# Kernel optimization log

Hardware: AMD Instinct MI355X
Metric: run time of the kernel (lower is better)

## Reference

```python
import jax, jax.numpy as jnp
import numpy as np
from math import sqrt

B, L, S, H, E = 4, 2048, 2048, 16, 64


def setup_inputs() -> dict:
    key = jax.random.key(0)
    kq, kk, kv = jax.random.split(key, 3)
    queries = jax.random.normal(kq, (B, L, H, E), dtype=jnp.float32)
    keys = jax.random.normal(kk, (B, S, H, E), dtype=jnp.float32)
    values = jax.random.normal(kv, (B, S, H, E), dtype=jnp.float32)
    # causal mask: True where attention is disallowed (upper triangle, excl diag)
    causal = jnp.triu(jnp.ones((L, S), dtype=jnp.bool_), k=1)
    attention_mask = jnp.broadcast_to(causal[None, None, :, :], (B, 1, L, S))
    return {"queries": queries, "keys": keys, "values": values,
            "attention_mask": attention_mask}


def reference(queries, keys, values, attention_mask):
    E_ = queries.shape[-1]
    scale = 1.0 / sqrt(E_)
    # [B,H,L,S] full score matrix (the quadratic intermediate of naive attention)
    scores = jnp.einsum('blhe,bshe->bhls', queries, keys)
    scores = jnp.where(attention_mask, -jnp.inf, scores)
    A = jnp.nan_to_num(jax.nn.softmax(scale * scores, axis=-1))
    V = jnp.einsum('bhls,bshd->blhd', A, values)
    return V
```

## Files before the change

kernel.cpp:

```cpp
#include <hip/hip_runtime.h>
#include <cmath>

#define B_ 4
#define L_ 2048
#define S_ 2048
#define H_ 16
#define E_ 64
#define SCALE 0.125f

typedef __attribute__((ext_vector_type(4))) float f32x4;
typedef __attribute__((ext_vector_type(8))) __bf16 bf16x8;
typedef __attribute__((ext_vector_type(8))) unsigned short ushort8;
typedef __attribute__((ext_vector_type(4))) unsigned short ushort4v;
union FragU { ushort8 u; bf16x8 b; };

__device__ __forceinline__ unsigned short f2bf(float f) {
    unsigned int u = __float_as_uint(f);
    return (unsigned short)((u + 0x7FFFu + ((u >> 16) & 1u)) >> 16);
}

__device__ __forceinline__ void gload_lds16(const void* g, void* l) {
    __builtin_amdgcn_global_load_lds(
        (const __attribute__((address_space(1))) void*)g,
        (__attribute__((address_space(3))) void*)l, 16, 0, 0);
}

__global__ __launch_bounds__(256) void conv_k(const float* __restrict__ K,
                                              unsigned short* __restrict__ Kbf) {
    const int idx = blockIdx.x * 256 + threadIdx.x;
    const int j   = idx & 7;
    const int row = idx >> 3;
    const int s   = row & (S_ - 1);
    const int bh  = row >> 11;
    const int h   = bh & (H_ - 1);
    const int b   = bh >> 4;
    const int jp  = j ^ (s & 7);
    const float* src = K + (((size_t)b * S_ + s) * H_ + h) * E_ + jp * 8;
    f32x4 a = *(const f32x4*)src;
    f32x4 d = *(const f32x4*)(src + 4);
    ushort8 u;
    u[0]=f2bf(a[0]); u[1]=f2bf(a[1]); u[2]=f2bf(a[2]); u[3]=f2bf(a[3]);
    u[4]=f2bf(d[0]); u[5]=f2bf(d[1]); u[6]=f2bf(d[2]); u[7]=f2bf(d[3]);
    *(ushort8*)(Kbf + (size_t)row * E_ + j * 8) = u;
}

__global__ __launch_bounds__(256) void conv_v(const float* __restrict__ V,
                                              unsigned short* __restrict__ Vt) {
    __shared__ unsigned short t[64 * 72];
    const int tid  = threadIdx.x;
    const int sblk = blockIdx.x & 31;
    const int h    = (blockIdx.x >> 5) & 15;
    const int b    = blockIdx.x >> 9;
    const int s0   = sblk * 64;
    for (int i = 0; i < 4; ++i) {
        const int c = tid + i * 256;
        const int sr = c >> 4, e0 = (c & 15) * 4;
        f32x4 a = *(const f32x4*)(V + (((size_t)b * S_ + s0 + sr) * H_ + h) * E_ + e0);
        ushort4v u;
        u[0]=f2bf(a[0]); u[1]=f2bf(a[1]); u[2]=f2bf(a[2]); u[3]=f2bf(a[3]);
        *(ushort4v*)&t[sr * 72 + e0] = u;
    }
    __syncthreads();
    for (int i = 0; i < 2; ++i) {
        const int c = tid + i * 256;
        const int e = c >> 3, lc = c & 7, sch = lc ^ (e & 7);
        ushort8 u;
        for (int k = 0; k < 8; ++k) u[k] = t[(sch * 8 + k) * 72 + e];
        *(ushort8*)(Vt + ((size_t)(b * H_ + h) * E_ + e) * S_ + s0 + lc * 8) = u;
    }
}

template <bool PRE>
__global__ __launch_bounds__(256, 6) void fattn_kernel(
    const float* __restrict__ Q, const unsigned short* __restrict__ Kbf,
    const unsigned short* __restrict__ Vt, const float* __restrict__ Kf,
    const float* __restrict__ Vf, float* __restrict__ Out)
{
    const int tid  = threadIdx.x;
    const int wave = tid >> 6;
    const int lane = tid & 63;
    const int ln   = lane & 15;
    const int quad = lane >> 4;
    const int qtile = gridDim.x - 1 - blockIdx.x;
    const int h = blockIdx.y;
    const int b = blockIdx.z;
    const int q0 = qtile * 64;
    const int qw = q0 + wave * 16;
    const int p7 = ln & 7;

    __shared__ __align__(16) unsigned short ldsK[64 * 64];
    __shared__ __align__(16) unsigned short ldsV[64 * 64];
    __shared__ __align__(16) unsigned short ldsP[4][16 * 72];

    FragU qf[2];
    {
        const float* qp = Q + (((size_t)b * L_ + (qw + ln)) * H_ + h) * E_;
        for (int c = 0; c < 2; ++c) {
            const int e0 = c * 32 + quad * 8;
            f32x4 lo = *(const f32x4*)(qp + e0);
            f32x4 hi = *(const f32x4*)(qp + e0 + 4);
            ushort8 u;
            u[0]=f2bf(lo[0]*SCALE); u[1]=f2bf(lo[1]*SCALE);
            u[2]=f2bf(lo[2]*SCALE); u[3]=f2bf(lo[3]*SCALE);
            u[4]=f2bf(hi[0]*SCALE); u[5]=f2bf(hi[1]*SCALE);
            u[6]=f2bf(hi[2]*SCALE); u[7]=f2bf(hi[3]*SCALE);
            qf[c].u = u;
        }
    }

    f32x4 o[4];
    for (int et = 0; et < 4; ++et) o[et] = f32x4{0.f, 0.f, 0.f, 0.f};
    float l_r[4] = {0.f, 0.f, 0.f, 0.f};

    const unsigned short* kbh = Kbf + (size_t)(b * H_ + h) * S_ * E_;
    const unsigned short* vbh = Vt  + (size_t)(b * H_ + h) * E_ * S_;
    const float* kf32 = Kf + (((size_t)b * S_) * H_ + h) * E_;
    const float* vf32 = Vf + (((size_t)b * S_) * H_ + h) * E_;

    const int ntiles = qtile + 1;
    for (int kt = 0; kt < ntiles; ++kt) {
        const int k0 = kt * 64;
        __syncthreads();

        if constexpr (PRE) {
            const unsigned short* ktb = kbh + (size_t)k0 * E_;
            const unsigned short* vtb = vbh + k0;
            for (int i = 0; i < 2; ++i) {
                const int slot0 = wave * 128 + i * 64;
                gload_lds16(ktb + (size_t)(slot0 + lane) * 8, &ldsK[slot0 * 8]);
            }
            for (int i = 0; i < 2; ++i) {
                const int slot0 = wave * 128 + i * 64;
                const int slot  = slot0 + lane;
                const int e = slot >> 3, lc = slot & 7;
                gload_lds16(vtb + (size_t)e * S_ + lc * 8, &ldsV[slot0 * 8]);
            }
        } else {
            for (int i = 0; i < 2; ++i) {
                const int c = tid + i * 256;
                const int key = c >> 3, j = c & 7, jp = j ^ (key & 7);
                const float* src = kf32 + (size_t)(k0 + key) * (H_ * E_) + jp * 8;
                f32x4 a = *(const f32x4*)src, d = *(const f32x4*)(src + 4);
                ushort8 u;
                u[0]=f2bf(a[0]); u[1]=f2bf(a[1]); u[2]=f2bf(a[2]); u[3]=f2bf(a[3]);
                u[4]=f2bf(d[0]); u[5]=f2bf(d[1]); u[6]=f2bf(d[2]); u[7]=f2bf(d[3]);
                *(ushort8*)&ldsK[key * 64 + j * 8] = u;
            }
            for (int i = 0; i < 2; ++i) {
                const int c = tid + i * 256;
                const int e = c >> 3, lc = c & 7, sch = lc ^ (e & 7);
                ushort8 u;
                for (int t = 0; t < 8; ++t)
                    u[t] = f2bf(vf32[(size_t)(k0 + sch * 8 + t) * (H_ * E_) + e]);
                *(ushort8*)&ldsV[e * 64 + lc * 8] = u;
            }
        }
        __syncthreads();

        f32x4 sfr[4];
        for (int n = 0; n < 4; ++n) {
            FragU kf0, kf1;
            kf0.u = *(const ushort8*)&ldsK[(n*16+ln)*64 + ((quad    ) ^ p7) * 8];
            kf1.u = *(const ushort8*)&ldsK[(n*16+ln)*64 + ((4 + quad) ^ p7) * 8];
            f32x4 acc = f32x4{0.f, 0.f, 0.f, 0.f};
            acc = __builtin_amdgcn_mfma_f32_16x16x32_bf16(qf[0].b, kf0.b, acc, 0, 0, 0);
            acc = __builtin_amdgcn_mfma_f32_16x16x32_bf16(qf[1].b, kf1.b, acc, 0, 0, 0);
            sfr[n] = acc;
        }

        for (int r = 0; r < 4; ++r) {
            const int qrow = qw + quad * 4 + r;
            for (int n = 0; n < 4; ++n) {
                const int col = k0 + n * 16 + ln;
                float p = __expf(sfr[n][r]);
                p = (col <= qrow) ? p : 0.f;
                l_r[r] += p;
                ldsP[wave][(quad * 4 + r) * 72 + n * 16 + ln] = f2bf(p);
            }
        }

        FragU pf0, pf1;
        pf0.u = *(const ushort8*)&ldsP[wave][ln * 72 + quad * 8];
        pf1.u = *(const ushort8*)&ldsP[wave][ln * 72 + 32 + quad * 8];
        for (int et = 0; et < 4; ++et) {
            FragU vf0, vf1;
            vf0.u = *(const ushort8*)&ldsV[(et*16+ln)*64 + ((quad    ) ^ p7) * 8];
            vf1.u = *(const ushort8*)&ldsV[(et*16+ln)*64 + ((4 + quad) ^ p7) * 8];
            o[et] = __builtin_amdgcn_mfma_f32_16x16x32_bf16(pf0.b, vf0.b, o[et], 0, 0, 0);
            o[et] = __builtin_amdgcn_mfma_f32_16x16x32_bf16(pf1.b, vf1.b, o[et], 0, 0, 0);
        }
    }

    for (int r = 0; r < 4; ++r) {
        float s = l_r[r];
        s += __shfl_xor(s, 1); s += __shfl_xor(s, 2);
        s += __shfl_xor(s, 4); s += __shfl_xor(s, 8);
        l_r[r] = s;
    }

    for (int r = 0; r < 4; ++r) {
        const float inv = 1.f / l_r[r];
        const int qrow = qw + quad * 4 + r;
        float* op = Out + (((size_t)b * L_ + qrow) * H_ + h) * E_;
        for (int et = 0; et < 4; ++et)
            op[et * 16 + ln] = o[et][r] * inv;
    }
}

extern "C" void kernel_launch(void* const* d_in, const int* in_sizes, int n_in,
                              void* d_out, int out_size, void* d_ws, size_t ws_size,
                              hipStream_t stream) {
    const float* Q = (const float*)d_in[0];
    const float* K = (const float*)d_in[1];
    const float* V = (const float*)d_in[2];
    float* Out = (float*)d_out;

    const size_t plane = (size_t)B_ * H_ * S_ * E_;
    unsigned short* Kbf = (unsigned short*)d_ws;
    unsigned short* Vt  = Kbf + plane;

    dim3 grid(L_ / 64, H_, B_);
    if (ws_size >= plane * 2 * sizeof(unsigned short)) {
        conv_k<<<(int)(plane / 8 / 256), 256, 0, stream>>>(K, Kbf);
        conv_v<<<B_ * H_ * (S_ / 64), 256, 0, stream>>>(V, Vt);
        fattn_kernel<true><<<grid, dim3(256), 0, stream>>>(Q, Kbf, Vt, K, V, Out);
    } else {
        fattn_kernel<false><<<grid, dim3(256), 0, stream>>>(Q, Kbf, Vt, K, V, Out);
    }
}
```

Baseline: 277.7 us.

## Double-buffer K tiles in LDS and load V fragments directly from global

K tiles are now prefetched into a double-buffered LDS array one tile ahead, which removes one of the two barriers per iteration. V fragments are read straight from global memory into registers instead of being staged through LDS, so the V transpose kernel drops its XOR swizzle. Softmax now uses exp2 with log2(e) folded into the Q scale, and the occupancy hint drops from 6 to 4 waves per SIMD to allow more registers. The direct global V loads are strided and repeated by every wave, and correctness relies on the asynchronous LDS loads finishing before the barrier.

```diff
diff --git a/kernel.cpp b/kernel.cpp
--- a/kernel.cpp
+++ b/kernel.cpp
@@ -6,7 +6,7 @@
 #define S_ 2048
 #define H_ 16
 #define E_ 64
-#define SCALE 0.125f
+#define SCALE2 0.18033688011112042f
 
 typedef __attribute__((ext_vector_type(4))) float f32x4;
 typedef __attribute__((ext_vector_type(8))) __bf16 bf16x8;
@@ -46,7 +46,7 @@
 
 __global__ __launch_bounds__(256) void conv_v(const float* __restrict__ V,
                                               unsigned short* __restrict__ Vt) {
-    __shared__ unsigned short t[64 * 72];
+    __shared__ unsigned short t[64 * 65];
     const int tid  = threadIdx.x;
     const int sblk = blockIdx.x & 31;
     const int h    = (blockIdx.x >> 5) & 15;
@@ -56,22 +56,23 @@
         const int c = tid + i * 256;
         const int sr = c >> 4, e0 = (c & 15) * 4;
         f32x4 a = *(const f32x4*)(V + (((size_t)b * S_ + s0 + sr) * H_ + h) * E_ + e0);
-        ushort4v u;
-        u[0]=f2bf(a[0]); u[1]=f2bf(a[1]); u[2]=f2bf(a[2]); u[3]=f2bf(a[3]);
-        *(ushort4v*)&t[sr * 72 + e0] = u;
+        t[sr * 65 + e0 + 0] = f2bf(a[0]);
+        t[sr * 65 + e0 + 1] = f2bf(a[1]);
+        t[sr * 65 + e0 + 2] = f2bf(a[2]);
+        t[sr * 65 + e0 + 3] = f2bf(a[3]);
     }
     __syncthreads();
     for (int i = 0; i < 2; ++i) {
         const int c = tid + i * 256;
-        const int e = c >> 3, lc = c & 7, sch = lc ^ (e & 7);
+        const int e = c >> 3, lc = c & 7;
         ushort8 u;
-        for (int k = 0; k < 8; ++k) u[k] = t[(sch * 8 + k) * 72 + e];
+        for (int k = 0; k < 8; ++k) u[k] = t[(lc * 8 + k) * 65 + e];
         *(ushort8*)(Vt + ((size_t)(b * H_ + h) * E_ + e) * S_ + s0 + lc * 8) = u;
     }
 }
 
 template <bool PRE>
-__global__ __launch_bounds__(256, 6) void fattn_kernel(
+__global__ __launch_bounds__(256, 4) void fattn_kernel(
     const float* __restrict__ Q, const unsigned short* __restrict__ Kbf,
     const unsigned short* __restrict__ Vt, const float* __restrict__ Kf,
     const float* __restrict__ Vf, float* __restrict__ Out)
@@ -88,8 +89,7 @@
     const int qw = q0 + wave * 16;
     const int p7 = ln & 7;
 
-    __shared__ __align__(16) unsigned short ldsK[64 * 64];
-    __shared__ __align__(16) unsigned short ldsV[64 * 64];
+    __shared__ __align__(16) unsigned short kbuf[2][64 * 64];
     __shared__ __align__(16) unsigned short ldsP[4][16 * 72];
 
     FragU qf[2];
@@ -100,10 +100,10 @@
             f32x4 lo = *(const f32x4*)(qp + e0);
             f32x4 hi = *(const f32x4*)(qp + e0 + 4);
             ushort8 u;
-            u[0]=f2bf(lo[0]*SCALE); u[1]=f2bf(lo[1]*SCALE);
-            u[2]=f2bf(lo[2]*SCALE); u[3]=f2bf(lo[3]*SCALE);
-            u[4]=f2bf(hi[0]*SCALE); u[5]=f2bf(hi[1]*SCALE);
-            u[6]=f2bf(hi[2]*SCALE); u[7]=f2bf(hi[3]*SCALE);
+            u[0]=f2bf(lo[0]*SCALE2); u[1]=f2bf(lo[1]*SCALE2);
+            u[2]=f2bf(lo[2]*SCALE2); u[3]=f2bf(lo[3]*SCALE2);
+            u[4]=f2bf(hi[0]*SCALE2); u[5]=f2bf(hi[1]*SCALE2);
+            u[6]=f2bf(hi[2]*SCALE2); u[7]=f2bf(hi[3]*SCALE2);
             qf[c].u = u;
         }
     }
@@ -118,23 +118,35 @@
     const float* vf32 = Vf + (((size_t)b * S_) * H_ + h) * E_;
 
     const int ntiles = qtile + 1;
+
+    if constexpr (PRE) {
+        const unsigned short* ktb = kbh;
+        for (int i = 0; i < 2; ++i) {
+            const int slot0 = wave * 128 + i * 64;
+            gload_lds16(ktb + (size_t)(slot0 + lane) * 8, &kbuf[0][slot0 * 8]);
+        }
+    }
+
     for (int kt = 0; kt < ntiles; ++kt) {
         const int k0 = kt * 64;
         __syncthreads();
 
+        FragU vf[4][2];
+        const unsigned short* kb;
         if constexpr (PRE) {
-            const unsigned short* ktb = kbh + (size_t)k0 * E_;
-            const unsigned short* vtb = vbh + k0;
-            for (int i = 0; i < 2; ++i) {
-                const int slot0 = wave * 128 + i * 64;
-                gload_lds16(ktb + (size_t)(slot0 + lane) * 8, &ldsK[slot0 * 8]);
-            }
-            for (int i = 0; i < 2; ++i) {
-                const int slot0 = wave * 128 + i * 64;
-                const int slot  = slot0 + lane;
-                const int e = slot >> 3, lc = slot & 7;
-                gload_lds16(vtb + (size_t)e * S_ + lc * 8, &ldsV[slot0 * 8]);
-            }
+            if (kt + 1 < ntiles) {
+                const unsigned short* ktb = kbh + (size_t)(k0 + 64) * E_;
+                unsigned short* dst = kbuf[(kt + 1) & 1];
+                for (int i = 0; i < 2; ++i) {
+                    const int slot0 = wave * 128 + i * 64;
+                    gload_lds16(ktb + (size_t)(slot0 + lane) * 8, &dst[slot0 * 8]);
+                }
+            }
+            for (int et = 0; et < 4; ++et)
+                for (int hf = 0; hf < 2; ++hf)
+                    vf[et][hf].u = *(const ushort8*)(
+                        vbh + (size_t)(et * 16 + ln) * S_ + k0 + hf * 32 + quad * 8);
+            kb = kbuf[kt & 1];
         } else {
             for (int i = 0; i < 2; ++i) {
                 const int c = tid + i * 256;
@@ -144,24 +156,33 @@
                 ushort8 u;
                 u[0]=f2bf(a[0]); u[1]=f2bf(a[1]); u[2]=f2bf(a[2]); u[3]=f2bf(a[3]);
                 u[4]=f2bf(d[0]); u[5]=f2bf(d[1]); u[6]=f2bf(d[2]); u[7]=f2bf(d[3]);
-                *(ushort8*)&ldsK[key * 64 + j * 8] = u;
-            }
-            for (int i = 0; i < 2; ++i) {
-                const int c = tid + i * 256;
-                const int e = c >> 3, lc = c & 7, sch = lc ^ (e & 7);
-                ushort8 u;
-                for (int t = 0; t < 8; ++t)
-                    u[t] = f2bf(vf32[(size_t)(k0 + sch * 8 + t) * (H_ * E_) + e]);
-                *(ushort8*)&ldsV[e * 64 + lc * 8] = u;
-            }
-        }
-        __syncthreads();
+                *(ushort8*)&kbuf[0][key * 64 + j * 8] = u;
+            }
+            {
+                const int s = tid & 63;
+                const int eb = (tid >> 6) * 16;
+                const float* vp = vf32 + (size_t)(k0 + s) * (H_ * E_) + eb;
+                for (int i = 0; i < 4; ++i) {
+                    f32x4 v4 = *(const f32x4*)(vp + i * 4);
+                    kbuf[1][(eb + i * 4 + 0) * 64 + s] = f2bf(v4[0]);
+                    kbuf[1][(eb + i * 4 + 1) * 64 + s] = f2bf(v4[1]);
+                    kbuf[1][(eb + i * 4 + 2) * 64 + s] = f2bf(v4[2]);
+                    kbuf[1][(eb + i * 4 + 3) * 64 + s] = f2bf(v4[3]);
+                }
+            }
+            __syncthreads();
+            for (int et = 0; et < 4; ++et)
+                for (int hf = 0; hf < 2; ++hf)
+                    vf[et][hf].u = *(const ushort8*)
+                        &kbuf[1][(et * 16 + ln) * 64 + hf * 32 + quad * 8];
+            kb = kbuf[0];
+        }
 
         f32x4 sfr[4];
         for (int n = 0; n < 4; ++n) {
             FragU kf0, kf1;
-            kf0.u = *(const ushort8*)&ldsK[(n*16+ln)*64 + ((quad    ) ^ p7) * 8];
-            kf1.u = *(const ushort8*)&ldsK[(n*16+ln)*64 + ((4 + quad) ^ p7) * 8];
+            kf0.u = *(const ushort8*)&kb[(n*16+ln)*64 + ((quad    ) ^ p7) * 8];
+            kf1.u = *(const ushort8*)&kb[(n*16+ln)*64 + ((4 + quad) ^ p7) * 8];
             f32x4 acc = f32x4{0.f, 0.f, 0.f, 0.f};
             acc = __builtin_amdgcn_mfma_f32_16x16x32_bf16(qf[0].b, kf0.b, acc, 0, 0, 0);
             acc = __builtin_amdgcn_mfma_f32_16x16x32_bf16(qf[1].b, kf1.b, acc, 0, 0, 0);
@@ -172,7 +193,7 @@
             const int qrow = qw + quad * 4 + r;
             for (int n = 0; n < 4; ++n) {
                 const int col = k0 + n * 16 + ln;
-                float p = __expf(sfr[n][r]);
+                float p = __builtin_exp2f(sfr[n][r]);
                 p = (col <= qrow) ? p : 0.f;
                 l_r[r] += p;
                 ldsP[wave][(quad * 4 + r) * 72 + n * 16 + ln] = f2bf(p);
@@ -183,11 +204,8 @@
         pf0.u = *(const ushort8*)&ldsP[wave][ln * 72 + quad * 8];
         pf1.u = *(const ushort8*)&ldsP[wave][ln * 72 + 32 + quad * 8];
         for (int et = 0; et < 4; ++et) {
-            FragU vf0, vf1;
-            vf0.u = *(const ushort8*)&ldsV[(et*16+ln)*64 + ((quad    ) ^ p7) * 8];
-            vf1.u = *(const ushort8*)&ldsV[(et*16+ln)*64 + ((4 + quad) ^ p7) * 8];
-            o[et] = __builtin_amdgcn_mfma_f32_16x16x32_bf16(pf0.b, vf0.b, o[et], 0, 0, 0);
-            o[et] = __builtin_amdgcn_mfma_f32_16x16x32_bf16(pf1.b, vf1.b, o[et], 0, 0, 0);
+            o[et] = __builtin_amdgcn_mfma_f32_16x16x32_bf16(pf0.b, vf[et][0].b, o[et], 0, 0, 0);
+            o[et] = __builtin_amdgcn_mfma_f32_16x16x32_bf16(pf1.b, vf[et][1].b, o[et], 0, 0, 0);
         }
     }
 
@@ -197,7 +215,6 @@
         s += __shfl_xor(s, 4); s += __shfl_xor(s, 8);
         l_r[r] = s;
     }
-
     for (int r = 0; r < 4; ++r) {
         const float inv = 1.f / l_r[r];
         const int qrow = qw + quad * 4 + r;
```

Result: slower. 427.3 us (+53.9%).

## Enlarge query tile to 128 rows per block and skip fully-masked tiles

Applied to the files above, without the earlier changes.

Each wave now handles 32 query rows, so each block covers 128 queries and every K/V tile loaded into LDS is reused by twice as many rows. Waves skip key tiles that lie entirely above their causal diagonal and apply the mask only on diagonal tiles. Softmax uses exp2 with the log2(e) factor folded into the Q scale, and the row sum accumulates the bf16-truncated probabilities so it matches the values fed to the PV matmul. The grid is halved with occupancy lowered to 4 blocks per CU, which risks less latency hiding and more imbalance across waves within a block; the V transpose buffer padding was also changed.

```diff
diff --git a/kernel.cpp b/kernel.cpp
--- a/kernel.cpp
+++ b/kernel.cpp
@@ -6,12 +6,11 @@
 #define S_ 2048
 #define H_ 16
 #define E_ 64
-#define SCALE 0.125f
+#define SCALE2 0.18033688011112042f
 
 typedef __attribute__((ext_vector_type(4))) float f32x4;
 typedef __attribute__((ext_vector_type(8))) __bf16 bf16x8;
 typedef __attribute__((ext_vector_type(8))) unsigned short ushort8;
-typedef __attribute__((ext_vector_type(4))) unsigned short ushort4v;
 union FragU { ushort8 u; bf16x8 b; };
 
 __device__ __forceinline__ unsigned short f2bf(float f) {
@@ -46,7 +45,7 @@
 
 __global__ __launch_bounds__(256) void conv_v(const float* __restrict__ V,
                                               unsigned short* __restrict__ Vt) {
-    __shared__ unsigned short t[64 * 72];
+    __shared__ unsigned short t[64 * 65];
     const int tid  = threadIdx.x;
     const int sblk = blockIdx.x & 31;
     const int h    = (blockIdx.x >> 5) & 15;
@@ -56,22 +55,23 @@
         const int c = tid + i * 256;
         const int sr = c >> 4, e0 = (c & 15) * 4;
         f32x4 a = *(const f32x4*)(V + (((size_t)b * S_ + s0 + sr) * H_ + h) * E_ + e0);
-        ushort4v u;
-        u[0]=f2bf(a[0]); u[1]=f2bf(a[1]); u[2]=f2bf(a[2]); u[3]=f2bf(a[3]);
-        *(ushort4v*)&t[sr * 72 + e0] = u;
+        t[sr * 65 + e0 + 0] = f2bf(a[0]);
+        t[sr * 65 + e0 + 1] = f2bf(a[1]);
+        t[sr * 65 + e0 + 2] = f2bf(a[2]);
+        t[sr * 65 + e0 + 3] = f2bf(a[3]);
     }
     __syncthreads();
     for (int i = 0; i < 2; ++i) {
         const int c = tid + i * 256;
         const int e = c >> 3, lc = c & 7, sch = lc ^ (e & 7);
         ushort8 u;
-        for (int k = 0; k < 8; ++k) u[k] = t[(sch * 8 + k) * 72 + e];
+        for (int k = 0; k < 8; ++k) u[k] = t[(sch * 8 + k) * 65 + e];
         *(ushort8*)(Vt + ((size_t)(b * H_ + h) * E_ + e) * S_ + s0 + lc * 8) = u;
     }
 }
 
 template <bool PRE>
-__global__ __launch_bounds__(256, 6) void fattn_kernel(
+__global__ __launch_bounds__(256, 4) void fattn_kernel(
     const float* __restrict__ Q, const unsigned short* __restrict__ Kbf,
     const unsigned short* __restrict__ Vt, const float* __restrict__ Kf,
     const float* __restrict__ Vf, float* __restrict__ Out)
@@ -84,40 +84,41 @@
     const int qtile = gridDim.x - 1 - blockIdx.x;
     const int h = blockIdx.y;
     const int b = blockIdx.z;
-    const int q0 = qtile * 64;
-    const int qw = q0 + wave * 16;
+    const int q0 = qtile * 128;
+    const int qw = q0 + wave * 32;
     const int p7 = ln & 7;
 
     __shared__ __align__(16) unsigned short ldsK[64 * 64];
     __shared__ __align__(16) unsigned short ldsV[64 * 64];
-    __shared__ __align__(16) unsigned short ldsP[4][16 * 72];
-
-    FragU qf[2];
-    {
-        const float* qp = Q + (((size_t)b * L_ + (qw + ln)) * H_ + h) * E_;
+    __shared__ __align__(16) unsigned short ldsP[4][32 * 72];
+
+    FragU qf[2][2];
+    for (int rs = 0; rs < 2; ++rs) {
+        const float* qp = Q + (((size_t)b * L_ + (qw + rs * 16 + ln)) * H_ + h) * E_;
         for (int c = 0; c < 2; ++c) {
             const int e0 = c * 32 + quad * 8;
             f32x4 lo = *(const f32x4*)(qp + e0);
             f32x4 hi = *(const f32x4*)(qp + e0 + 4);
             ushort8 u;
-            u[0]=f2bf(lo[0]*SCALE); u[1]=f2bf(lo[1]*SCALE);
-            u[2]=f2bf(lo[2]*SCALE); u[3]=f2bf(lo[3]*SCALE);
-            u[4]=f2bf(hi[0]*SCALE); u[5]=f2bf(hi[1]*SCALE);
-            u[6]=f2bf(hi[2]*SCALE); u[7]=f2bf(hi[3]*SCALE);
-            qf[c].u = u;
-        }
-    }
-
-    f32x4 o[4];
-    for (int et = 0; et < 4; ++et) o[et] = f32x4{0.f, 0.f, 0.f, 0.f};
-    float l_r[4] = {0.f, 0.f, 0.f, 0.f};
+            u[0]=f2bf(lo[0]*SCALE2); u[1]=f2bf(lo[1]*SCALE2);
+            u[2]=f2bf(lo[2]*SCALE2); u[3]=f2bf(lo[3]*SCALE2);
+            u[4]=f2bf(hi[0]*SCALE2); u[5]=f2bf(hi[1]*SCALE2);
+            u[6]=f2bf(hi[2]*SCALE2); u[7]=f2bf(hi[3]*SCALE2);
+            qf[rs][c].u = u;
+        }
+    }
+
+    f32x4 o[2][4];
+    for (int rs = 0; rs < 2; ++rs)
+        for (int et = 0; et < 4; ++et) o[rs][et] = f32x4{0.f, 0.f, 0.f, 0.f};
+    float l_r[2][4] = {{0.f,0.f,0.f,0.f},{0.f,0.f,0.f,0.f}};
 
     const unsigned short* kbh = Kbf + (size_t)(b * H_ + h) * S_ * E_;
     const unsigned short* vbh = Vt  + (size_t)(b * H_ + h) * E_ * S_;
     const float* kf32 = Kf + (((size_t)b * S_) * H_ + h) * E_;
     const float* vf32 = Vf + (((size_t)b * S_) * H_ + h) * E_;
 
-    const int ntiles = qtile + 1;
+    const int ntiles = 2 * qtile + 2;
     for (int kt = 0; kt < ntiles; ++kt) {
         const int k0 = kt * 64;
         __syncthreads();
@@ -157,53 +158,66 @@
         }
         __syncthreads();
 
-        f32x4 sfr[4];
+        if (k0 > qw + 31) continue;
+        const bool need_mask = (k0 + 63 > qw);
+
+        f32x4 sfr[2][4];
         for (int n = 0; n < 4; ++n) {
             FragU kf0, kf1;
             kf0.u = *(const ushort8*)&ldsK[(n*16+ln)*64 + ((quad    ) ^ p7) * 8];
             kf1.u = *(const ushort8*)&ldsK[(n*16+ln)*64 + ((4 + quad) ^ p7) * 8];
-            f32x4 acc = f32x4{0.f, 0.f, 0.f, 0.f};
-            acc = __builtin_amdgcn_mfma_f32_16x16x32_bf16(qf[0].b, kf0.b, acc, 0, 0, 0);
-            acc = __builtin_amdgcn_mfma_f32_16x16x32_bf16(qf[1].b, kf1.b, acc, 0, 0, 0);
-            sfr[n] = acc;
-        }
-
-        for (int r = 0; r < 4; ++r) {
-            const int qrow = qw + quad * 4 + r;
-            for (int n = 0; n < 4; ++n) {
-                const int col = k0 + n * 16 + ln;
-                float p = __expf(sfr[n][r]);
-                p = (col <= qrow) ? p : 0.f;
-                l_r[r] += p;
-                ldsP[wave][(quad * 4 + r) * 72 + n * 16 + ln] = f2bf(p);
-            }
-        }
-
-        FragU pf0, pf1;
-        pf0.u = *(const ushort8*)&ldsP[wave][ln * 72 + quad * 8];
-        pf1.u = *(const ushort8*)&ldsP[wave][ln * 72 + 32 + quad * 8];
+            for (int rs = 0; rs < 2; ++rs) {
+                f32x4 acc = f32x4{0.f, 0.f, 0.f, 0.f};
+                acc = __builtin_amdgcn_mfma_f32_16x16x32_bf16(qf[rs][0].b, kf0.b, acc, 0, 0, 0);
+                acc = __builtin_amdgcn_mfma_f32_16x16x32_bf16(qf[rs][1].b, kf1.b, acc, 0, 0, 0);
+                sfr[rs][n] = acc;
+            }
+        }
+
+        for (int rs = 0; rs < 2; ++rs) {
+            for (int r = 0; r < 4; ++r) {
+                const int qrow = qw + rs * 16 + quad * 4 + r;
+                for (int n = 0; n < 4; ++n) {
+                    float p = __builtin_exp2f(sfr[rs][n][r]);
+                    if (need_mask) {
+                        const int col = k0 + n * 16 + ln;
+                        p = (col <= qrow) ? p : 0.f;
+                    }
+                    const unsigned int u = __float_as_uint(p) & 0xFFFF0000u;
+                    l_r[rs][r] += __uint_as_float(u);
+                    ldsP[wave][(rs * 16 + quad * 4 + r) * 72 + n * 16 + ln] =
+                        (unsigned short)(u >> 16);
+                }
+            }
+        }
+
+        FragU pf[2][2];
+        for (int rs = 0; rs < 2; ++rs) {
+            pf[rs][0].u = *(const ushort8*)&ldsP[wave][(rs*16+ln) * 72 + quad * 8];
+            pf[rs][1].u = *(const ushort8*)&ldsP[wave][(rs*16+ln) * 72 + 32 + quad * 8];
+        }
         for (int et = 0; et < 4; ++et) {
             FragU vf0, vf1;
             vf0.u = *(const ushort8*)&ldsV[(et*16+ln)*64 + ((quad    ) ^ p7) * 8];
             vf1.u = *(const ushort8*)&ldsV[(et*16+ln)*64 + ((4 + quad) ^ p7) * 8];
-            o[et] = __builtin_amdgcn_mfma_f32_16x16x32_bf16(pf0.b, vf0.b, o[et], 0, 0, 0);
-            o[et] = __builtin_amdgcn_mfma_f32_16x16x32_bf16(pf1.b, vf1.b, o[et], 0, 0, 0);
-        }
-    }
-
-    for (int r = 0; r < 4; ++r) {
-        float s = l_r[r];
-        s += __shfl_xor(s, 1); s += __shfl_xor(s, 2);
-        s += __shfl_xor(s, 4); s += __shfl_xor(s, 8);
-        l_r[r] = s;
-    }
-
-    for (int r = 0; r < 4; ++r) {
-        const float inv = 1.f / l_r[r];
-        const int qrow = qw + quad * 4 + r;
-        float* op = Out + (((size_t)b * L_ + qrow) * H_ + h) * E_;
-        for (int et = 0; et < 4; ++et)
-            op[et * 16 + ln] = o[et][r] * inv;
+            for (int rs = 0; rs < 2; ++rs) {
+                o[rs][et] = __builtin_amdgcn_mfma_f32_16x16x32_bf16(pf[rs][0].b, vf0.b, o[rs][et], 0, 0, 0);
+                o[rs][et] = __builtin_amdgcn_mfma_f32_16x16x32_bf16(pf[rs][1].b, vf1.b, o[rs][et], 0, 0, 0);
+            }
+        }
+    }
+
+    for (int rs = 0; rs < 2; ++rs) {
+        for (int r = 0; r < 4; ++r) {
+            float s = l_r[rs][r];
+            s += __shfl_xor(s, 1); s += __shfl_xor(s, 2);
+            s += __shfl_xor(s, 4); s += __shfl_xor(s, 8);
+            const float inv = 1.f / s;
+            const int qrow = qw + rs * 16 + quad * 4 + r;
+            float* op = Out + (((size_t)b * L_ + qrow) * H_ + h) * E_;
+            for (int et = 0; et < 4; ++et)
+                op[et * 16 + ln] = o[rs][et][r] * inv;
+        }
     }
 }
 
@@ -219,7 +233,7 @@
     unsigned short* Kbf = (unsigned short*)d_ws;
     unsigned short* Vt  = Kbf + plane;
 
-    dim3 grid(L_ / 64, H_, B_);
+    dim3 grid(L_ / 128, H_, B_);
     if (ws_size >= plane * 2 * sizeof(unsigned short)) {
         conv_k<<<(int)(plane / 8 / 256), 256, 0, stream>>>(K, Kbf);
         conv_v<<<B_ * H_ * (S_ / 64), 256, 0, stream>>>(V, Vt);
```

Result: no change. 283.1 us (+2.0%).

## Keep softmax probabilities in registers via transposed QK^T MFMA and permuted V layout

Applied to the files above, without the earlier changes.

Swaps the MFMA operands so the score fragment comes out transposed: each lane holds keys for a single query row. The probabilities can then be packed straight into bf16 A-fragments in registers, which removes the per-wave LDS round trip for P. To match the new key ordering, V is stored in a permuted key order both in the conversion kernel and in the in-kernel fallback. The change also folds log2(e) into the Q scale so exp2 can be used, applies the causal mask only on the diagonal tile, keeps one row-sum per lane, and lowers the occupancy hint from 6 to 4 blocks. The bf16 pack truncates instead of rounding, and the lower occupancy hint may reduce latency hiding.

```diff
diff --git a/kernel.cpp b/kernel.cpp
--- a/kernel.cpp
+++ b/kernel.cpp
@@ -6,17 +6,21 @@
 #define S_ 2048
 #define H_ 16
 #define E_ 64
-#define SCALE 0.125f
+#define SCALE2 0.18033688011112042f
 
 typedef __attribute__((ext_vector_type(4))) float f32x4;
 typedef __attribute__((ext_vector_type(8))) __bf16 bf16x8;
 typedef __attribute__((ext_vector_type(8))) unsigned short ushort8;
-typedef __attribute__((ext_vector_type(4))) unsigned short ushort4v;
-union FragU { ushort8 u; bf16x8 b; };
+union FragU { ushort8 u; bf16x8 b; unsigned int d[4]; };
 
 __device__ __forceinline__ unsigned short f2bf(float f) {
     unsigned int u = __float_as_uint(f);
     return (unsigned short)((u + 0x7FFFu + ((u >> 16) & 1u)) >> 16);
+}
+
+__device__ __forceinline__ unsigned int pack_bf(float hi, float lo) {
+    return __builtin_amdgcn_perm(__float_as_uint(hi), __float_as_uint(lo),
+                                 0x07060302u);
 }
 
 __device__ __forceinline__ void gload_lds16(const void* g, void* l) {
@@ -46,7 +50,7 @@
 
 __global__ __launch_bounds__(256) void conv_v(const float* __restrict__ V,
                                               unsigned short* __restrict__ Vt) {
-    __shared__ unsigned short t[64 * 72];
+    __shared__ unsigned short t[64 * 65];
     const int tid  = threadIdx.x;
     const int sblk = blockIdx.x & 31;
     const int h    = (blockIdx.x >> 5) & 15;
@@ -56,22 +60,29 @@
         const int c = tid + i * 256;
         const int sr = c >> 4, e0 = (c & 15) * 4;
         f32x4 a = *(const f32x4*)(V + (((size_t)b * S_ + s0 + sr) * H_ + h) * E_ + e0);
-        ushort4v u;
-        u[0]=f2bf(a[0]); u[1]=f2bf(a[1]); u[2]=f2bf(a[2]); u[3]=f2bf(a[3]);
-        *(ushort4v*)&t[sr * 72 + e0] = u;
+        t[sr * 65 + e0 + 0] = f2bf(a[0]);
+        t[sr * 65 + e0 + 1] = f2bf(a[1]);
+        t[sr * 65 + e0 + 2] = f2bf(a[2]);
+        t[sr * 65 + e0 + 3] = f2bf(a[3]);
     }
     __syncthreads();
     for (int i = 0; i < 2; ++i) {
-        const int c = tid + i * 256;
-        const int e = c >> 3, lc = c & 7, sch = lc ^ (e & 7);
+        const int c  = tid + i * 256;
+        const int e  = c >> 3, cc = c & 7;
+        const int q  = cc >> 1, half = cc & 1;
         ushort8 u;
-        for (int k = 0; k < 8; ++k) u[k] = t[(sch * 8 + k) * 72 + e];
-        *(ushort8*)(Vt + ((size_t)(b * H_ + h) * E_ + e) * S_ + s0 + lc * 8) = u;
+        for (int j = 0; j < 8; ++j) {
+            const int d = j >> 2, r = j & 3;
+            const int key = (2 * half + d) * 16 + q * 4 + r;
+            u[j] = t[key * 65 + e];
+        }
+        *(ushort8*)(Vt + ((size_t)(b * H_ + h) * E_ + e) * S_ + s0
+                    + (cc ^ (e & 7)) * 8) = u;
     }
 }
 
 template <bool PRE>
-__global__ __launch_bounds__(256, 6) void fattn_kernel(
+__global__ __launch_bounds__(256, 4) void fattn_kernel(
     const float* __restrict__ Q, const unsigned short* __restrict__ Kbf,
     const unsigned short* __restrict__ Vt, const float* __restrict__ Kf,
     const float* __restrict__ Vf, float* __restrict__ Out)
@@ -87,10 +98,10 @@
     const int q0 = qtile * 64;
     const int qw = q0 + wave * 16;
     const int p7 = ln & 7;
+    const int qrow = qw + ln;
 
     __shared__ __align__(16) unsigned short ldsK[64 * 64];
     __shared__ __align__(16) unsigned short ldsV[64 * 64];
-    __shared__ __align__(16) unsigned short ldsP[4][16 * 72];
 
     FragU qf[2];
     {
@@ -100,17 +111,17 @@
             f32x4 lo = *(const f32x4*)(qp + e0);
             f32x4 hi = *(const f32x4*)(qp + e0 + 4);
             ushort8 u;
-            u[0]=f2bf(lo[0]*SCALE); u[1]=f2bf(lo[1]*SCALE);
-            u[2]=f2bf(lo[2]*SCALE); u[3]=f2bf(lo[3]*SCALE);
-            u[4]=f2bf(hi[0]*SCALE); u[5]=f2bf(hi[1]*SCALE);
-            u[6]=f2bf(hi[2]*SCALE); u[7]=f2bf(hi[3]*SCALE);
+            u[0]=f2bf(lo[0]*SCALE2); u[1]=f2bf(lo[1]*SCALE2);
+            u[2]=f2bf(lo[2]*SCALE2); u[3]=f2bf(lo[3]*SCALE2);
+            u[4]=f2bf(hi[0]*SCALE2); u[5]=f2bf(hi[1]*SCALE2);
+            u[6]=f2bf(hi[2]*SCALE2); u[7]=f2bf(hi[3]*SCALE2);
             qf[c].u = u;
         }
     }
 
     f32x4 o[4];
     for (int et = 0; et < 4; ++et) o[et] = f32x4{0.f, 0.f, 0.f, 0.f};
-    float l_r[4] = {0.f, 0.f, 0.f, 0.f};
+    float lsum = 0.f;
 
     const unsigned short* kbh = Kbf + (size_t)(b * H_ + h) * S_ * E_;
     const unsigned short* vbh = Vt  + (size_t)(b * H_ + h) * E_ * S_;
@@ -148,11 +159,15 @@
             }
             for (int i = 0; i < 2; ++i) {
                 const int c = tid + i * 256;
-                const int e = c >> 3, lc = c & 7, sch = lc ^ (e & 7);
+                const int e = c >> 3, cc = c & 7;
+                const int q = cc >> 1, half = cc & 1;
                 ushort8 u;
-                for (int t = 0; t < 8; ++t)
-                    u[t] = f2bf(vf32[(size_t)(k0 + sch * 8 + t) * (H_ * E_) + e]);
-                *(ushort8*)&ldsV[e * 64 + lc * 8] = u;
+                for (int j = 0; j < 8; ++j) {
+                    const int d = j >> 2, r = j & 3;
+                    const int key = (2 * half + d) * 16 + q * 4 + r;
+                    u[j] = f2bf(vf32[(size_t)(k0 + key) * (H_ * E_) + e]);
+                }
+                *(ushort8*)&ldsV[e * 64 + (cc ^ (e & 7)) * 8] = u;
             }
         }
         __syncthreads();
@@ -163,47 +178,52 @@
             kf0.u = *(const ushort8*)&ldsK[(n*16+ln)*64 + ((quad    ) ^ p7) * 8];
             kf1.u = *(const ushort8*)&ldsK[(n*16+ln)*64 + ((4 + quad) ^ p7) * 8];
             f32x4 acc = f32x4{0.f, 0.f, 0.f, 0.f};
-            acc = __builtin_amdgcn_mfma_f32_16x16x32_bf16(qf[0].b, kf0.b, acc, 0, 0, 0);
-            acc = __builtin_amdgcn_mfma_f32_16x16x32_bf16(qf[1].b, kf1.b, acc, 0, 0, 0);
+            acc = __builtin_amdgcn_mfma_f32_16x16x32_bf16(kf0.b, qf[0].b, acc, 0, 0, 0);
+            acc = __builtin_amdgcn_mfma_f32_16x16x32_bf16(kf1.b, qf[1].b, acc, 0, 0, 0);
             sfr[n] = acc;
         }
 
-        for (int r = 0; r < 4; ++r) {
-            const int qrow = qw + quad * 4 + r;
-            for (int n = 0; n < 4; ++n) {
-                const int col = k0 + n * 16 + ln;
-                float p = __expf(sfr[n][r]);
-                p = (col <= qrow) ? p : 0.f;
-                l_r[r] += p;
-                ldsP[wave][(quad * 4 + r) * 72 + n * 16 + ln] = f2bf(p);
-            }
-        }
-
+        const bool need_mask = (kt == qtile);
+        unsigned int pk[4][2];
+        for (int n = 0; n < 4; ++n) {
+            float p[4];
+            for (int r = 0; r < 4; ++r) {
+                float v = __builtin_exp2f(sfr[n][r]);
+                if (need_mask) {
+                    const int key = k0 + n * 16 + quad * 4 + r;
+                    v = (key <= qrow) ? v : 0.f;
+                }
+                lsum += v;
+                p[r] = v;
+            }
+            pk[n][0] = pack_bf(p[1], p[0]);
+            pk[n][1] = pack_bf(p[3], p[2]);
+        }
         FragU pf0, pf1;
-        pf0.u = *(const ushort8*)&ldsP[wave][ln * 72 + quad * 8];
-        pf1.u = *(const ushort8*)&ldsP[wave][ln * 72 + 32 + quad * 8];
+        pf0.d[0] = pk[0][0]; pf0.d[1] = pk[0][1];
+        pf0.d[2] = pk[1][0]; pf0.d[3] = pk[1][1];
+        pf1.d[0] = pk[2][0]; pf1.d[1] = pk[2][1];
+        pf1.d[2] = pk[3][0]; pf1.d[3] = pk[3][1];
+
         for (int et = 0; et < 4; ++et) {
             FragU vf0, vf1;
-            vf0.u = *(const ushort8*)&ldsV[(et*16+ln)*64 + ((quad    ) ^ p7) * 8];
-            vf1.u = *(const ushort8*)&ldsV[(et*16+ln)*64 + ((4 + quad) ^ p7) * 8];
+            vf0.u = *(const ushort8*)&ldsV[(et*16+ln)*64 + ((2*quad    ) ^ p7) * 8];
+            vf1.u = *(const ushort8*)&ldsV[(et*16+ln)*64 + ((2*quad + 1) ^ p7) * 8];
             o[et] = __builtin_amdgcn_mfma_f32_16x16x32_bf16(pf0.b, vf0.b, o[et], 0, 0, 0);
             o[et] = __builtin_amdgcn_mfma_f32_16x16x32_bf16(pf1.b, vf1.b, o[et], 0, 0, 0);
         }
     }
 
+    lsum += __shfl_xor(lsum, 16);
+    lsum += __shfl_xor(lsum, 32);
+    const float inv = 1.f / lsum;
+
     for (int r = 0; r < 4; ++r) {
-        float s = l_r[r];
-        s += __shfl_xor(s, 1); s += __shfl_xor(s, 2);
-        s += __shfl_xor(s, 4); s += __shfl_xor(s, 8);
-        l_r[r] = s;
-    }
-
-    for (int r = 0; r < 4; ++r) {
-        const float inv = 1.f / l_r[r];
-        const int qrow = qw + quad * 4 + r;
-        float* op = Out + (((size_t)b * L_ + qrow) * H_ + h) * E_;
+        const int row = quad * 4 + r;
+        const float invr = __shfl(inv, row);
+        float* op = Out + (((size_t)b * L_ + (qw + row)) * H_ + h) * E_;
         for (int et = 0; et < 4; ++et)
-            op[et * 16 + ln] = o[et][r] * inv;
+            op[et * 16 + ln] = o[et][r] * invr;
     }
 }
 
```

Result: faster. 257.7 us (-7.2%).
